# Kernel optimization log

Measured on AMD Instinct MI355X. Metric: run time of the kernel, lower is better.

## Reference

```python
import jax, jax.numpy as jnp
import numpy as np

B, D, FV, EMB, HID, E = 256, 1000, 300, 128, 128, 32000
NUM_LAYERS = 3


def _gcn_layer(h, src, tgt, W, b):
    # PyG GCNConv (add_self_loops=True, normalize=True) over N = h.shape[0] nodes.
    # NOTE: edges only reference nodes [0, D) (faithful to original forward),
    # but self-loops exist for all N nodes.
    N = h.shape[0]
    h = h @ W.T  # [N, out]
    deg = jnp.ones((N,), h.dtype).at[tgt].add(1.0)  # self-loop + in-degree
    dinv = deg ** -0.5
    coef = dinv[src] * dinv[tgt]  # [E]
    agg = jnp.zeros_like(h).at[tgt].add(h[src] * coef[:, None])
    agg = agg + h * (dinv * dinv)[:, None]  # self-loop messages
    return agg + b


def setup_inputs() -> dict:
    key = jax.random.key(0)
    ks = jax.random.split(key, 10)
    inp = {
        "X_num": jax.random.normal(ks[0], (B, 800), jnp.float32),
        "X_cat": jax.random.normal(ks[1], (B, 200), jnp.float32),
        "V": jax.random.normal(ks[2], (D, FV), jnp.float32),
        "edge_index": jax.random.randint(ks[3], (2, E), 0, D, jnp.int32),
        "W_embed": jax.random.normal(ks[4], (EMB, FV), jnp.float32) / np.sqrt(FV),
        "b_embed": jnp.zeros((EMB,), jnp.float32),
        "W0": jax.random.normal(ks[5], (HID, EMB), jnp.float32) / np.sqrt(EMB),
        "b0": jnp.zeros((HID,), jnp.float32),
        "W1": jax.random.normal(ks[6], (HID, HID), jnp.float32) / np.sqrt(HID),
        "b1": jnp.zeros((HID,), jnp.float32),
        "W2": jax.random.normal(ks[7], (HID, HID), jnp.float32) / np.sqrt(HID),
        "b2": jnp.zeros((HID,), jnp.float32),
    }
    return inp


def reference(X_num, X_cat, V, edge_index, W_embed, b_embed, W0, b0, W1, b1, W2, b2):
    x = jnp.concatenate([X_num, X_cat], axis=1)  # [B, D]
    emb = V @ W_embed.T + b_embed  # [D, EMB]
    h = x[:, :, None] * emb[None, :, :]  # [B, D, EMB]
    h = h.reshape(B * D, EMB)
    src, tgt = edge_index[0], edge_index[1]
    for W, b in ((W0, b0), (W1, b1), (W2, b2)):
        h = jax.nn.relu(_gcn_layer(h, src, tgt, W, b))
    h = h.reshape(B, D, HID)
    return h.mean(axis=1)  # conv_pool_method == 'mean'
```

## Files before the change

kernel.cpp:

```cpp
#include <hip/hip_runtime.h>
#include <hip/hip_bf16.h>

#define B_N 256
#define D_N 1000
#define H_N 128
#define E_N 32000
#define CAP 128

typedef unsigned int uint32;
typedef unsigned short u16;
typedef __attribute__((ext_vector_type(8))) short bf16x8;
typedef __attribute__((ext_vector_type(4))) float f32x4;

__device__ __forceinline__ u16 f2bf(float f) {
    union { float f; uint32 u; } v; v.f = f;
    return (u16)((v.u + 0x7fffu + ((v.u >> 16) & 1u)) >> 16);
}
__device__ __forceinline__ uint32 pk2(float lo, float hi) {
    __hip_bfloat162 h = __float22bfloat162_rn(make_float2(lo, hi));
    union { __hip_bfloat162 h; uint32 u; } v; v.h = h; return v.u;
}
__device__ __forceinline__ float asf(uint32 u) {
    union { uint32 u; float f; } v; v.u = u; return v.f;
}
__device__ __forceinline__ float rl(float x) { return x > 0.f ? x : 0.f; }

__device__ __forceinline__ void ld8g(const float* __restrict__ p, int kbase, float v[8]) {
    if (kbase + 8 <= 300) {
        float4 a = *(const float4*)p, b = *(const float4*)(p + 4);
        v[0] = a.x; v[1] = a.y; v[2] = a.z; v[3] = a.w;
        v[4] = b.x; v[5] = b.y; v[6] = b.z; v[7] = b.w;
    } else {
#pragma unroll
        for (int j = 0; j < 8; ++j) v[j] = (kbase + j < 300) ? p[j] : 0.f;
    }
}

__global__ void k_prep(const float* __restrict__ V, const float* __restrict__ W_embed,
                       const float* __restrict__ b_embed, const float* __restrict__ W0,
                       const float* __restrict__ Xn, const float* __restrict__ Xc,
                       const float* __restrict__ W1, const float* __restrict__ W2,
                       int* __restrict__ deg,
                       u16* __restrict__ w1h, u16* __restrict__ w2h,
                       u16* __restrict__ E1h, float* __restrict__ t0,
                       float* __restrict__ out) {
    __shared__ __align__(16) u16 sW0[128 * 128];
    __shared__ __align__(16) u16 sWc[128 * 64];
    __shared__ __align__(16) u16 sVc[32 * 64];
    __shared__ __align__(16) u16 sT[32 * 128];

    int bid = blockIdx.x, tid = threadIdx.x;
    if (bid >= 32) {
        if (bid < 96) {
            int i = (bid - 32) * 256 + tid;
            w1h[i] = f2bf(W1[i]); w2h[i] = f2bf(W2[i]);
        } else if (bid < 224) {
            int i = (bid - 96) * 256 + tid;
            out[i] = 0.f;
        } else {
            for (int j = tid; j < D_N; j += 256) deg[j] = 0;
        }
        return;
    }

    const int wave = tid >> 6, lane = tid & 63;
    const int quad = lane >> 4, l15 = lane & 15;
    const int mt = wave & 1, nh = wave >> 1;
    const int dbase = bid * 32;

#pragma unroll
    for (int ii = 0; ii < 8; ++ii) {
        int idx = tid + ii * 256;
        int row = idx >> 4, g = idx & 15;
        float4 a = *(const float4*)(W0 + row * 128 + g * 8);
        float4 b = *(const float4*)(W0 + row * 128 + g * 8 + 4);
        uint4 pk = { pk2(a.x, a.y), pk2(a.z, a.w), pk2(b.x, b.y), pk2(b.z, b.w) };
        *(uint4*)&sW0[row * 128 + ((g ^ (row & 7)) << 3)] = pk;
    }

    f32x4 accA[4];
#pragma unroll
    for (int n = 0; n < 4; ++n) { accA[n][0] = 0.f; accA[n][1] = 0.f; accA[n][2] = 0.f; accA[n][3] = 0.f; }

    for (int ck = 0; ck < 5; ++ck) {
        int k0 = ck * 64;
        {
            int row = tid >> 3, seg = tid & 7;
            int d = dbase + row; int dc = d < D_N ? d : D_N - 1;
            int kk = k0 + seg * 8;
            float v[8]; ld8g(V + dc * 300 + kk, kk, v);
            uint4 pk = { pk2(v[0], v[1]), pk2(v[2], v[3]), pk2(v[4], v[5]), pk2(v[6], v[7]) };
            *(uint4*)&sVc[row * 64 + ((seg ^ (row & 7)) << 3)] = pk;
        }
        {
            int row = tid >> 1, half = tid & 1;
#pragma unroll
            for (int gg = 0; gg < 4; ++gg) {
                int g = half * 4 + gg;
                int kk = k0 + g * 8;
                float v[8]; ld8g(W_embed + row * 300 + kk, kk, v);
                uint4 pk = { pk2(v[0], v[1]), pk2(v[2], v[3]), pk2(v[4], v[5]), pk2(v[6], v[7]) };
                *(uint4*)&sWc[row * 64 + ((g ^ (row & 7)) << 3)] = pk;
            }
        }
        __syncthreads();
#pragma unroll
        for (int ksb = 0; ksb < 2; ++ksb) {
            int g = ksb * 4 + quad;
            int ar = mt * 16 + l15;
            bf16x8 av = *(const bf16x8*)&sVc[ar * 64 + ((g ^ (ar & 7)) << 3)];
#pragma unroll
            for (int n = 0; n < 4; ++n) {
                int br = nh * 64 + n * 16 + l15;
                bf16x8 bv = *(const bf16x8*)&sWc[br * 64 + ((g ^ (br & 7)) << 3)];
                accA[n] = __builtin_amdgcn_mfma_f32_16x16x32_bf16(av, bv, accA[n], 0, 0, 0);
            }
        }
        __syncthreads();
    }

    {
        const int odd = l15 & 1;
#pragma unroll
        for (int n = 0; n < 4; ++n) {
            float bb = b_embed[nh * 64 + n * 16 + l15];
            float v0 = accA[n][0] + bb, v1 = accA[n][1] + bb;
            float v2 = accA[n][2] + bb, v3 = accA[n][3] + bb;
            float t0_ = __shfl_xor(v0, 1), t1_ = __shfl_xor(v1, 1);
            float t2_ = __shfl_xor(v2, 1), t3_ = __shfl_xor(v3, 1);
            float lo0 = odd ? t2_ : v0, hi0 = odd ? v2 : t0_;
            float lo1 = odd ? t3_ : v1, hi1 = odd ? v3 : t1_;
            int r0 = mt * 16 + quad * 4 + (odd ? 2 : 0);
            int r1 = r0 + 1;
            int ce = nh * 64 + n * 16 + (l15 & ~1);
            *(uint32*)&sT[r0 * 128 + (((ce >> 3) ^ (r0 & 7)) << 3) + (ce & 7)] = pk2(lo0, hi0);
            *(uint32*)&sT[r1 * 128 + (((ce >> 3) ^ (r1 & 7)) << 3) + (ce & 7)] = pk2(lo1, hi1);
        }
    }
    __syncthreads();

    f32x4 accB[4];
#pragma unroll
    for (int n = 0; n < 4; ++n) { accB[n][0] = 0.f; accB[n][1] = 0.f; accB[n][2] = 0.f; accB[n][3] = 0.f; }
#pragma unroll
    for (int ks = 0; ks < 4; ++ks) {
        int g = ks * 4 + quad;
        int ar = mt * 16 + l15;
        bf16x8 av = *(const bf16x8*)&sT[ar * 128 + ((g ^ (ar & 7)) << 3)];
#pragma unroll
        for (int n = 0; n < 4; ++n) {
            int br = nh * 64 + n * 16 + l15;
            bf16x8 bv = *(const bf16x8*)&sW0[br * 128 + ((g ^ (br & 7)) << 3)];
            accB[n] = __builtin_amdgcn_mfma_f32_16x16x32_bf16(av, bv, accB[n], 0, 0, 0);
        }
    }

#pragma unroll
    for (int i = 0; i < 4; ++i) {
        int r = mt * 16 + quad * 4 + i;
        int d = dbase + r;
        if (d < D_N) {
            float x0 = (d < 800) ? Xn[d] : Xc[d - 800];
#pragma unroll
            for (int n = 0; n < 4; ++n) {
                int col = nh * 64 + n * 16 + l15;
                float e1 = accB[n][i];
                E1h[d * H_N + col] = f2bf(e1);
                t0[d * H_N + col] = x0 * e1;
            }
        }
    }
}

__global__ void k_layer(const float* __restrict__ t_in, const float* __restrict__ bias,
                        const float* __restrict__ Wn, const int* __restrict__ deg,
                        const int* __restrict__ es,
                        float* __restrict__ t_out, float* out, int pool) {
    __shared__ float sh[128];
    int d = blockIdx.x, e = threadIdx.x;
    float di = rsqrtf(1.f + (float)deg[d]);
    float acc = t_in[d * H_N + e] * di * di;
    int n = deg[d]; if (n > CAP) n = CAP;
    const int* row = es + d * CAP;
    int i = 0;
    for (; i + 4 <= n; i += 4) {
        int a0 = row[i], a1 = row[i + 1], a2 = row[i + 2], a3 = row[i + 3];
        float c0 = rsqrtf(1.f + (float)deg[a0]);
        float c1 = rsqrtf(1.f + (float)deg[a1]);
        float c2 = rsqrtf(1.f + (float)deg[a2]);
        float c3 = rsqrtf(1.f + (float)deg[a3]);
        acc += di * (c0 * t_in[a0 * H_N + e] + c1 * t_in[a1 * H_N + e] +
                     c2 * t_in[a2 * H_N + e] + c3 * t_in[a3 * H_N + e]);
    }
    for (; i < n; ++i) {
        int s = row[i];
        acc += di * rsqrtf(1.f + (float)deg[s]) * t_in[s * H_N + e];
    }
    float h = rl(acc + bias[e]);
    if (pool) { atomicAdd(&out[e], h * (1.0f / 1000.0f)); return; }
    sh[e] = h;
    __syncthreads();
    const float4* hr = (const float4*)sh;
    const float4* wr = (const float4*)(Wn + e * 128);
    float s = 0.f;
#pragma unroll 8
    for (int k = 0; k < 32; ++k) {
        float4 a = hr[k], w = wr[k];
        s += a.x * w.x + a.y * w.y + a.z * w.z + a.w * w.w;
    }
    t_out[d * H_N + e] = s;
}

__global__ __launch_bounds__(256, 2)
void k_big(const float* __restrict__ Xn, const float* __restrict__ Xc,
           const u16* __restrict__ E1h, const u16* __restrict__ w1h,
           const u16* __restrict__ w2h, const float* __restrict__ b0,
           const float* __restrict__ b1, const float* __restrict__ b2,
           const int* __restrict__ eidx, int* __restrict__ deg,
           int* __restrict__ es, float* __restrict__ out) {
    __shared__ __align__(16) u16 sW[128 * 128];
    __shared__ __align__(16) u16 sH[4 * 32 * 128];

    if (blockIdx.x >= 2040) {
        int e = (blockIdx.x - 2040) * 256 + threadIdx.x;
        int s = eidx[e], t = eidx[E_N + e];
        int pos = atomicAdd(&deg[t], 1);
        if (pos < CAP) es[t * CAP + pos] = s;
        return;
    }

    const int tid = threadIdx.x;
    const int wave = tid >> 6, lane = tid & 63;
    const int quad = lane >> 4, l15 = lane & 15;
    const int bi = 1 + (blockIdx.x >> 3);
    const int d0 = (blockIdx.x & 7) << 7;
    u16* hw = sH + wave * (32 * 128);

    {
        const uint4* w1v = (const uint4*)w1h;
#pragma unroll
        for (int i = 0; i < 8; ++i) {
            int idx = tid + i * 256;
            int row = idx >> 4, g = idx & 15;
            *(uint4*)&sW[row * 128 + ((g ^ (row & 7)) << 3)] = w1v[idx];
        }
    }

    {
        float4 b0a = *(const float4*)(b0 + l15 * 8);
        float4 b0b = *(const float4*)(b0 + l15 * 8 + 4);
#pragma unroll
        for (int it = 0; it < 8; ++it) {
            int r32 = it * 4 + quad;
            int d = d0 + wave * 32 + r32;
            int dc = d < D_N ? d : D_N - 1;
            float xv = (dc < 800) ? Xn[bi * 800 + dc] : Xc[bi * 200 + dc - 800];
            uint4 eg = *(const uint4*)(E1h + dc * H_N + l15 * 8);
            float v0 = rl(fmaf(xv, asf(eg.x << 16), b0a.x));
            float v1 = rl(fmaf(xv, asf(eg.x & 0xffff0000u), b0a.y));
            float v2 = rl(fmaf(xv, asf(eg.y << 16), b0a.z));
            float v3 = rl(fmaf(xv, asf(eg.y & 0xffff0000u), b0a.w));
            float v4 = rl(fmaf(xv, asf(eg.z << 16), b0b.x));
            float v5 = rl(fmaf(xv, asf(eg.z & 0xffff0000u), b0b.y));
            float v6 = rl(fmaf(xv, asf(eg.w << 16), b0b.z));
            float v7 = rl(fmaf(xv, asf(eg.w & 0xffff0000u), b0b.w));
            uint4 pk = { pk2(v0, v1), pk2(v2, v3), pk2(v4, v5), pk2(v6, v7) };
            *(uint4*)&hw[r32 * 128 + ((l15 ^ (r32 & 7)) << 3)] = pk;
        }
    }

    float b1g[8], b2g[8];
#pragma unroll
    for (int n = 0; n < 8; ++n) { b1g[n] = b1[n * 16 + l15]; b2g[n] = b2[n * 16 + l15]; }

    __syncthreads();

    f32x4 acc[2][8];
#pragma unroll
    for (int rt = 0; rt < 2; ++rt)
#pragma unroll
        for (int n = 0; n < 8; ++n) {
            acc[rt][n][0] = 0.f; acc[rt][n][1] = 0.f;
            acc[rt][n][2] = 0.f; acc[rt][n][3] = 0.f;
        }

#pragma unroll
    for (int ks = 0; ks < 4; ++ks) {
        int k8 = ks * 4 + quad;
        int m0 = l15, m1 = 16 + l15;
        bf16x8 a0 = *(const bf16x8*)&hw[m0 * 128 + ((k8 ^ (m0 & 7)) << 3)];
        bf16x8 a1 = *(const bf16x8*)&hw[m1 * 128 + ((k8 ^ (m1 & 7)) << 3)];
#pragma unroll
        for (int n = 0; n < 8; ++n) {
            int br = n * 16 + l15;
            bf16x8 bw = *(const bf16x8*)&sW[br * 128 + ((k8 ^ (br & 7)) << 3)];
            acc[0][n] = __builtin_amdgcn_mfma_f32_16x16x32_bf16(a0, bw, acc[0][n], 0, 0, 0);
            acc[1][n] = __builtin_amdgcn_mfma_f32_16x16x32_bf16(a1, bw, acc[1][n], 0, 0, 0);
        }
    }

    {
        const int odd = l15 & 1;
#pragma unroll
        for (int rt = 0; rt < 2; ++rt)
#pragma unroll
            for (int n = 0; n < 8; ++n) {
                float v0 = rl(acc[rt][n][0] + b1g[n]);
                float v1 = rl(acc[rt][n][1] + b1g[n]);
                float v2 = rl(acc[rt][n][2] + b1g[n]);
                float v3 = rl(acc[rt][n][3] + b1g[n]);
                float t0_ = __shfl_xor(v0, 1), t1_ = __shfl_xor(v1, 1);
                float t2_ = __shfl_xor(v2, 1), t3_ = __shfl_xor(v3, 1);
                float lo0 = odd ? t2_ : v0, hi0 = odd ? v2 : t0_;
                float lo1 = odd ? t3_ : v1, hi1 = odd ? v3 : t1_;
                int r0 = rt * 16 + quad * 4 + (odd ? 2 : 0);
                int r1 = r0 + 1;
                int ce = n * 16 + (l15 & ~1);
                *(uint32*)&hw[r0 * 128 + (((ce >> 3) ^ (r0 & 7)) << 3) + (ce & 7)] = pk2(lo0, hi0);
                *(uint32*)&hw[r1 * 128 + (((ce >> 3) ^ (r1 & 7)) << 3) + (ce & 7)] = pk2(lo1, hi1);
            }
    }

#pragma unroll
    for (int rt = 0; rt < 2; ++rt)
#pragma unroll
        for (int n = 0; n < 8; ++n) {
            acc[rt][n][0] = 0.f; acc[rt][n][1] = 0.f;
            acc[rt][n][2] = 0.f; acc[rt][n][3] = 0.f;
        }
#pragma unroll
    for (int ks = 0; ks < 4; ++ks) {
        int k8 = ks * 4 + quad;
        int m0 = l15, m1 = 16 + l15;
        bf16x8 a0 = *(const bf16x8*)&hw[m0 * 128 + ((k8 ^ (m0 & 7)) << 3)];
        bf16x8 a1 = *(const bf16x8*)&hw[m1 * 128 + ((k8 ^ (m1 & 7)) << 3)];
#pragma unroll
        for (int n = 0; n < 8; ++n) {
            bf16x8 bw = *(const bf16x8*)(w2h + (n * 16 + l15) * H_N + k8 * 8);
            acc[0][n] = __builtin_amdgcn_mfma_f32_16x16x32_bf16(a0, bw, acc[0][n], 0, 0, 0);
            acc[1][n] = __builtin_amdgcn_mfma_f32_16x16x32_bf16(a1, bw, acc[1][n], 0, 0, 0);
        }
    }

    int rem = D_N - d0 - wave * 32;
#pragma unroll
    for (int n = 0; n < 8; ++n) {
        float cs = 0.f;
#pragma unroll
        for (int rt = 0; rt < 2; ++rt)
#pragma unroll
            for (int i = 0; i < 4; ++i) {
                int r32 = rt * 16 + quad * 4 + i;
                float v = rl(acc[rt][n][i] + b2g[n]);
                if (r32 < rem) cs += v;
            }
        cs += __shfl_xor(cs, 16);
        cs += __shfl_xor(cs, 32);
        if (lane < 16) atomicAdd(&out[bi * H_N + n * 16 + l15], cs * (1.0f / 1000.0f));
    }
}

extern "C" void kernel_launch(void* const* d_in, const int* in_sizes, int n_in,
                              void* d_out, int out_size, void* d_ws, size_t ws_size,
                              hipStream_t stream) {
    const float* Xn = (const float*)d_in[0];
    const float* Xc = (const float*)d_in[1];
    const float* V = (const float*)d_in[2];
    const int* eidx = (const int*)d_in[3];
    const float* W_embed = (const float*)d_in[4];
    const float* b_embed = (const float*)d_in[5];
    const float* W0 = (const float*)d_in[6];
    const float* b0 = (const float*)d_in[7];
    const float* W1 = (const float*)d_in[8];
    const float* b1 = (const float*)d_in[9];
    const float* W2 = (const float*)d_in[10];
    const float* b2 = (const float*)d_in[11];
    float* out = (float*)d_out;

    char* p = (char*)d_ws;
    auto alloc = [&](size_t bytes) -> char* {
        char* r = p;
        p += (bytes + 255) & ~(size_t)255;
        return r;
    };
    u16*   E1h = (u16*)  alloc(D_N * H_N * 2);
    float* t0  = (float*)alloc(D_N * H_N * 4);
    float* t1  = (float*)alloc(D_N * H_N * 4);
    float* t2  = (float*)alloc(D_N * H_N * 4);
    u16*   w1h = (u16*)  alloc(H_N * H_N * 2);
    u16*   w2h = (u16*)  alloc(H_N * H_N * 2);
    int*   deg = (int*)  alloc(D_N * 4);
    int*   es  = (int*)  alloc(D_N * CAP * 4);

    k_prep<<<dim3(225), dim3(256), 0, stream>>>(V, W_embed, b_embed, W0, Xn, Xc,
                                                W1, W2, deg, w1h, w2h, E1h, t0, out);
    k_big<<<dim3(2165), dim3(256), 0, stream>>>(Xn, Xc, E1h, w1h, w2h, b0, b1, b2,
                                                eidx, deg, es, out);
    k_layer<<<dim3(1000), dim3(128), 0, stream>>>(t0, b0, W1, deg, es, t1, out, 0);
    k_layer<<<dim3(1000), dim3(128), 0, stream>>>(t1, b1, W2, deg, es, t2, out, 0);
    k_layer<<<dim3(1000), dim3(128), 0, stream>>>(t2, b2, (const float*)nullptr, deg, es,
                                                  (float*)nullptr, out, 1);
}
```

Before: 202.4 us.

## Halve prep tile rows and drop shared W1 staging in k_big for occupancy

k_prep now handles 16 rows per block instead of 32, with each wave owning 32 output columns, so more blocks cover the embedding GEMM. k_big no longer stages W1 in shared memory or builds the first-layer activations in LDS. It computes the relu(x*E1+b0) A-fragments directly in registers and reads W1 fragments from global/L2, and its launch bounds rise to 4 blocks per SM. The edge-scatter blocks move to the front of the grid so their atomics start early. The cost is more global loads of weights per wave, plus possible register pressure under the tighter launch bound.

```diff
diff --git a/kernel.cpp b/kernel.cpp
--- a/kernel.cpp
+++ b/kernel.cpp
@@ -46,16 +46,16 @@
                        float* __restrict__ out) {
     __shared__ __align__(16) u16 sW0[128 * 128];
     __shared__ __align__(16) u16 sWc[128 * 64];
-    __shared__ __align__(16) u16 sVc[32 * 64];
-    __shared__ __align__(16) u16 sT[32 * 128];
+    __shared__ __align__(16) u16 sVc[16 * 64];
+    __shared__ __align__(16) u16 sT[16 * 128];
 
     int bid = blockIdx.x, tid = threadIdx.x;
-    if (bid >= 32) {
-        if (bid < 96) {
-            int i = (bid - 32) * 256 + tid;
+    if (bid >= 63) {
+        if (bid < 127) {
+            int i = (bid - 63) * 256 + tid;
             w1h[i] = f2bf(W1[i]); w2h[i] = f2bf(W2[i]);
-        } else if (bid < 224) {
-            int i = (bid - 96) * 256 + tid;
+        } else if (bid < 255) {
+            int i = (bid - 127) * 256 + tid;
             out[i] = 0.f;
         } else {
             for (int j = tid; j < D_N; j += 256) deg[j] = 0;
@@ -65,8 +65,8 @@
 
     const int wave = tid >> 6, lane = tid & 63;
     const int quad = lane >> 4, l15 = lane & 15;
-    const int mt = wave & 1, nh = wave >> 1;
-    const int dbase = bid * 32;
+    const int nh = wave;
+    const int dbase = bid * 16;
 
 #pragma unroll
     for (int ii = 0; ii < 8; ++ii) {
@@ -78,13 +78,13 @@
         *(uint4*)&sW0[row * 128 + ((g ^ (row & 7)) << 3)] = pk;
     }
 
-    f32x4 accA[4];
-#pragma unroll
-    for (int n = 0; n < 4; ++n) { accA[n][0] = 0.f; accA[n][1] = 0.f; accA[n][2] = 0.f; accA[n][3] = 0.f; }
+    f32x4 accA[2];
+#pragma unroll
+    for (int n = 0; n < 2; ++n) { accA[n][0] = 0.f; accA[n][1] = 0.f; accA[n][2] = 0.f; accA[n][3] = 0.f; }
 
     for (int ck = 0; ck < 5; ++ck) {
         int k0 = ck * 64;
-        {
+        if (tid < 128) {
             int row = tid >> 3, seg = tid & 7;
             int d = dbase + row; int dc = d < D_N ? d : D_N - 1;
             int kk = k0 + seg * 8;
@@ -92,26 +92,24 @@
             uint4 pk = { pk2(v[0], v[1]), pk2(v[2], v[3]), pk2(v[4], v[5]), pk2(v[6], v[7]) };
             *(uint4*)&sVc[row * 64 + ((seg ^ (row & 7)) << 3)] = pk;
         }
-        {
-            int row = tid >> 1, half = tid & 1;
-#pragma unroll
-            for (int gg = 0; gg < 4; ++gg) {
-                int g = half * 4 + gg;
-                int kk = k0 + g * 8;
-                float v[8]; ld8g(W_embed + row * 300 + kk, kk, v);
-                uint4 pk = { pk2(v[0], v[1]), pk2(v[2], v[3]), pk2(v[4], v[5]), pk2(v[6], v[7]) };
-                *(uint4*)&sWc[row * 64 + ((g ^ (row & 7)) << 3)] = pk;
-            }
+#pragma unroll
+        for (int gg = 0; gg < 4; ++gg) {
+            int idx = tid + gg * 256;
+            int row = idx >> 3, g = idx & 7;
+            int kk = k0 + g * 8;
+            float v[8]; ld8g(W_embed + row * 300 + kk, kk, v);
+            uint4 pk = { pk2(v[0], v[1]), pk2(v[2], v[3]), pk2(v[4], v[5]), pk2(v[6], v[7]) };
+            *(uint4*)&sWc[row * 64 + ((g ^ (row & 7)) << 3)] = pk;
         }
         __syncthreads();
 #pragma unroll
         for (int ksb = 0; ksb < 2; ++ksb) {
             int g = ksb * 4 + quad;
-            int ar = mt * 16 + l15;
+            int ar = l15;
             bf16x8 av = *(const bf16x8*)&sVc[ar * 64 + ((g ^ (ar & 7)) << 3)];
 #pragma unroll
-            for (int n = 0; n < 4; ++n) {
-                int br = nh * 64 + n * 16 + l15;
+            for (int n = 0; n < 2; ++n) {
+                int br = nh * 32 + n * 16 + l15;
                 bf16x8 bv = *(const bf16x8*)&sWc[br * 64 + ((g ^ (br & 7)) << 3)];
                 accA[n] = __builtin_amdgcn_mfma_f32_16x16x32_bf16(av, bv, accA[n], 0, 0, 0);
             }
@@ -122,34 +120,34 @@
     {
         const int odd = l15 & 1;
 #pragma unroll
-        for (int n = 0; n < 4; ++n) {
-            float bb = b_embed[nh * 64 + n * 16 + l15];
+        for (int n = 0; n < 2; ++n) {
+            float bb = b_embed[nh * 32 + n * 16 + l15];
             float v0 = accA[n][0] + bb, v1 = accA[n][1] + bb;
             float v2 = accA[n][2] + bb, v3 = accA[n][3] + bb;
             float t0_ = __shfl_xor(v0, 1), t1_ = __shfl_xor(v1, 1);
             float t2_ = __shfl_xor(v2, 1), t3_ = __shfl_xor(v3, 1);
             float lo0 = odd ? t2_ : v0, hi0 = odd ? v2 : t0_;
             float lo1 = odd ? t3_ : v1, hi1 = odd ? v3 : t1_;
-            int r0 = mt * 16 + quad * 4 + (odd ? 2 : 0);
+            int r0 = quad * 4 + (odd ? 2 : 0);
             int r1 = r0 + 1;
-            int ce = nh * 64 + n * 16 + (l15 & ~1);
+            int ce = nh * 32 + n * 16 + (l15 & ~1);
             *(uint32*)&sT[r0 * 128 + (((ce >> 3) ^ (r0 & 7)) << 3) + (ce & 7)] = pk2(lo0, hi0);
             *(uint32*)&sT[r1 * 128 + (((ce >> 3) ^ (r1 & 7)) << 3) + (ce & 7)] = pk2(lo1, hi1);
         }
     }
     __syncthreads();
 
-    f32x4 accB[4];
-#pragma unroll
-    for (int n = 0; n < 4; ++n) { accB[n][0] = 0.f; accB[n][1] = 0.f; accB[n][2] = 0.f; accB[n][3] = 0.f; }
+    f32x4 accB[2];
+#pragma unroll
+    for (int n = 0; n < 2; ++n) { accB[n][0] = 0.f; accB[n][1] = 0.f; accB[n][2] = 0.f; accB[n][3] = 0.f; }
 #pragma unroll
     for (int ks = 0; ks < 4; ++ks) {
         int g = ks * 4 + quad;
-        int ar = mt * 16 + l15;
+        int ar = l15;
         bf16x8 av = *(const bf16x8*)&sT[ar * 128 + ((g ^ (ar & 7)) << 3)];
 #pragma unroll
-        for (int n = 0; n < 4; ++n) {
-            int br = nh * 64 + n * 16 + l15;
+        for (int n = 0; n < 2; ++n) {
+            int br = nh * 32 + n * 16 + l15;
             bf16x8 bv = *(const bf16x8*)&sW0[br * 128 + ((g ^ (br & 7)) << 3)];
             accB[n] = __builtin_amdgcn_mfma_f32_16x16x32_bf16(av, bv, accB[n], 0, 0, 0);
         }
@@ -157,13 +155,13 @@
 
 #pragma unroll
     for (int i = 0; i < 4; ++i) {
-        int r = mt * 16 + quad * 4 + i;
+        int r = quad * 4 + i;
         int d = dbase + r;
         if (d < D_N) {
             float x0 = (d < 800) ? Xn[d] : Xc[d - 800];
 #pragma unroll
-            for (int n = 0; n < 4; ++n) {
-                int col = nh * 64 + n * 16 + l15;
+            for (int n = 0; n < 2; ++n) {
+                int col = nh * 32 + n * 16 + l15;
                 float e1 = accB[n][i];
                 E1h[d * H_N + col] = f2bf(e1);
                 t0[d * H_N + col] = x0 * e1;
@@ -211,69 +209,34 @@
     t_out[d * H_N + e] = s;
 }
 
-__global__ __launch_bounds__(256, 2)
+__global__ __launch_bounds__(256, 4)
 void k_big(const float* __restrict__ Xn, const float* __restrict__ Xc,
            const u16* __restrict__ E1h, const u16* __restrict__ w1h,
            const u16* __restrict__ w2h, const float* __restrict__ b0,
            const float* __restrict__ b1, const float* __restrict__ b2,
            const int* __restrict__ eidx, int* __restrict__ deg,
            int* __restrict__ es, float* __restrict__ out) {
-    __shared__ __align__(16) u16 sW[128 * 128];
     __shared__ __align__(16) u16 sH[4 * 32 * 128];
 
-    if (blockIdx.x >= 2040) {
-        int e = (blockIdx.x - 2040) * 256 + threadIdx.x;
+    if (blockIdx.x < 125) {
+        int e = blockIdx.x * 256 + threadIdx.x;
         int s = eidx[e], t = eidx[E_N + e];
         int pos = atomicAdd(&deg[t], 1);
         if (pos < CAP) es[t * CAP + pos] = s;
         return;
     }
-
+    const int cb = blockIdx.x - 125;
     const int tid = threadIdx.x;
     const int wave = tid >> 6, lane = tid & 63;
     const int quad = lane >> 4, l15 = lane & 15;
-    const int bi = 1 + (blockIdx.x >> 3);
-    const int d0 = (blockIdx.x & 7) << 7;
+    const int bi = 1 + (cb >> 3);
+    const int mbase = ((cb & 7) << 7) + wave * 32;
     u16* hw = sH + wave * (32 * 128);
 
-    {
-        const uint4* w1v = (const uint4*)w1h;
-#pragma unroll
-        for (int i = 0; i < 8; ++i) {
-            int idx = tid + i * 256;
-            int row = idx >> 4, g = idx & 15;
-            *(uint4*)&sW[row * 128 + ((g ^ (row & 7)) << 3)] = w1v[idx];
-        }
-    }
-
-    {
-        float4 b0a = *(const float4*)(b0 + l15 * 8);
-        float4 b0b = *(const float4*)(b0 + l15 * 8 + 4);
-#pragma unroll
-        for (int it = 0; it < 8; ++it) {
-            int r32 = it * 4 + quad;
-            int d = d0 + wave * 32 + r32;
-            int dc = d < D_N ? d : D_N - 1;
-            float xv = (dc < 800) ? Xn[bi * 800 + dc] : Xc[bi * 200 + dc - 800];
-            uint4 eg = *(const uint4*)(E1h + dc * H_N + l15 * 8);
-            float v0 = rl(fmaf(xv, asf(eg.x << 16), b0a.x));
-            float v1 = rl(fmaf(xv, asf(eg.x & 0xffff0000u), b0a.y));
-            float v2 = rl(fmaf(xv, asf(eg.y << 16), b0a.z));
-            float v3 = rl(fmaf(xv, asf(eg.y & 0xffff0000u), b0a.w));
-            float v4 = rl(fmaf(xv, asf(eg.z << 16), b0b.x));
-            float v5 = rl(fmaf(xv, asf(eg.z & 0xffff0000u), b0b.y));
-            float v6 = rl(fmaf(xv, asf(eg.w << 16), b0b.z));
-            float v7 = rl(fmaf(xv, asf(eg.w & 0xffff0000u), b0b.w));
-            uint4 pk = { pk2(v0, v1), pk2(v2, v3), pk2(v4, v5), pk2(v6, v7) };
-            *(uint4*)&hw[r32 * 128 + ((l15 ^ (r32 & 7)) << 3)] = pk;
-        }
-    }
-
-    float b1g[8], b2g[8];
-#pragma unroll
-    for (int n = 0; n < 8; ++n) { b1g[n] = b1[n * 16 + l15]; b2g[n] = b2[n * 16 + l15]; }
-
-    __syncthreads();
+    const int rA = mbase + l15;  const int rAc = rA < D_N ? rA : D_N - 1;
+    const int rB = rA + 16;      const int rBc = rB < D_N ? rB : D_N - 1;
+    const float xvA = (rAc < 800) ? Xn[bi * 800 + rAc] : Xc[bi * 200 + rAc - 800];
+    const float xvB = (rBc < 800) ? Xn[bi * 800 + rBc] : Xc[bi * 200 + rBc - 800];
 
     f32x4 acc[2][8];
 #pragma unroll
@@ -286,16 +249,39 @@
 
 #pragma unroll
     for (int ks = 0; ks < 4; ++ks) {
-        int k8 = ks * 4 + quad;
-        int m0 = l15, m1 = 16 + l15;
-        bf16x8 a0 = *(const bf16x8*)&hw[m0 * 128 + ((k8 ^ (m0 & 7)) << 3)];
-        bf16x8 a1 = *(const bf16x8*)&hw[m1 * 128 + ((k8 ^ (m1 & 7)) << 3)];
+        const int k8 = ks * 4 + quad;
+        uint4 eA = *(const uint4*)(E1h + rAc * H_N + k8 * 8);
+        uint4 eB = *(const uint4*)(E1h + rBc * H_N + k8 * 8);
+        float4 bl = *(const float4*)(b0 + k8 * 8);
+        float4 bh = *(const float4*)(b0 + k8 * 8 + 4);
+        uint4 pA, pB;
+        {
+            float a0 = rl(fmaf(xvA, asf(eA.x << 16), bl.x));
+            float a1 = rl(fmaf(xvA, asf(eA.x & 0xffff0000u), bl.y));
+            float a2 = rl(fmaf(xvA, asf(eA.y << 16), bl.z));
+            float a3 = rl(fmaf(xvA, asf(eA.y & 0xffff0000u), bl.w));
+            float a4 = rl(fmaf(xvA, asf(eA.z << 16), bh.x));
+            float a5 = rl(fmaf(xvA, asf(eA.z & 0xffff0000u), bh.y));
+            float a6 = rl(fmaf(xvA, asf(eA.w << 16), bh.z));
+            float a7 = rl(fmaf(xvA, asf(eA.w & 0xffff0000u), bh.w));
+            pA = { pk2(a0, a1), pk2(a2, a3), pk2(a4, a5), pk2(a6, a7) };
+            float c0 = rl(fmaf(xvB, asf(eB.x << 16), bl.x));
+            float c1 = rl(fmaf(xvB, asf(eB.x & 0xffff0000u), bl.y));
+            float c2 = rl(fmaf(xvB, asf(eB.y << 16), bl.z));
+            float c3 = rl(fmaf(xvB, asf(eB.y & 0xffff0000u), bl.w));
+            float c4 = rl(fmaf(xvB, asf(eB.z << 16), bh.x));
+            float c5 = rl(fmaf(xvB, asf(eB.z & 0xffff0000u), bh.y));
+            float c6 = rl(fmaf(xvB, asf(eB.w << 16), bh.z));
+            float c7 = rl(fmaf(xvB, asf(eB.w & 0xffff0000u), bh.w));
+            pB = { pk2(c0, c1), pk2(c2, c3), pk2(c4, c5), pk2(c6, c7) };
+        }
+        bf16x8 aA = *(const bf16x8*)&pA;
+        bf16x8 aB = *(const bf16x8*)&pB;
 #pragma unroll
         for (int n = 0; n < 8; ++n) {
-            int br = n * 16 + l15;
-            bf16x8 bw = *(const bf16x8*)&sW[br * 128 + ((k8 ^ (br & 7)) << 3)];
-            acc[0][n] = __builtin_amdgcn_mfma_f32_16x16x32_bf16(a0, bw, acc[0][n], 0, 0, 0);
-            acc[1][n] = __builtin_amdgcn_mfma_f32_16x16x32_bf16(a1, bw, acc[1][n], 0, 0, 0);
+            bf16x8 bw = *(const bf16x8*)(w1h + (n * 16 + l15) * H_N + k8 * 8);
+            acc[0][n] = __builtin_amdgcn_mfma_f32_16x16x32_bf16(aA, bw, acc[0][n], 0, 0, 0);
+            acc[1][n] = __builtin_amdgcn_mfma_f32_16x16x32_bf16(aB, bw, acc[1][n], 0, 0, 0);
         }
     }
 
@@ -305,10 +291,11 @@
         for (int rt = 0; rt < 2; ++rt)
 #pragma unroll
             for (int n = 0; n < 8; ++n) {
-                float v0 = rl(acc[rt][n][0] + b1g[n]);
-                float v1 = rl(acc[rt][n][1] + b1g[n]);
-                float v2 = rl(acc[rt][n][2] + b1g[n]);
-                float v3 = rl(acc[rt][n][3] + b1g[n]);
+                float bg = b1[n * 16 + l15];
+                float v0 = rl(acc[rt][n][0] + bg);
+                float v1 = rl(acc[rt][n][1] + bg);
+                float v2 = rl(acc[rt][n][2] + bg);
+                float v3 = rl(acc[rt][n][3] + bg);
                 float t0_ = __shfl_xor(v0, 1), t1_ = __shfl_xor(v1, 1);
                 float t2_ = __shfl_xor(v2, 1), t3_ = __shfl_xor(v3, 1);
                 float lo0 = odd ? t2_ : v0, hi0 = odd ? v2 : t0_;
@@ -342,16 +329,17 @@
         }
     }
 
-    int rem = D_N - d0 - wave * 32;
+    int rem = D_N - mbase;
 #pragma unroll
     for (int n = 0; n < 8; ++n) {
+        float bg = b2[n * 16 + l15];
         float cs = 0.f;
 #pragma unroll
         for (int rt = 0; rt < 2; ++rt)
 #pragma unroll
             for (int i = 0; i < 4; ++i) {
                 int r32 = rt * 16 + quad * 4 + i;
-                float v = rl(acc[rt][n][i] + b2g[n]);
+                float v = rl(acc[rt][n][i] + bg);
                 if (r32 < rem) cs += v;
             }
         cs += __shfl_xor(cs, 16);
@@ -392,7 +380,7 @@
     int*   deg = (int*)  alloc(D_N * 4);
     int*   es  = (int*)  alloc(D_N * CAP * 4);
 
-    k_prep<<<dim3(225), dim3(256), 0, stream>>>(V, W_embed, b_embed, W0, Xn, Xc,
+    k_prep<<<dim3(256), dim3(256), 0, stream>>>(V, W_embed, b_embed, W0, Xn, Xc,
                                                 W1, W2, deg, w1h, w2h, E1h, t0, out);
     k_big<<<dim3(2165), dim3(256), 0, stream>>>(Xn, Xc, E1h, w1h, w2h, b0, b1, b2,
                                                 eidx, deg, es, out);
```

After: 226.4 us. +11.9%, slower.
